# Kernel tuning notes

Hardware: AMD Instinct MI355X
Metric: run time of the kernel (lower is better)

## Reference

```python
import jax, jax.numpy as jnp
import numpy as np

SEQ, B, IN, H, L = 512, 64, 512, 512, 2


def setup_inputs() -> dict:
    key = jax.random.key(0)
    ks = jax.random.split(key, 9)
    s = 0.02
    x = jax.random.normal(ks[0], (SEQ, B, IN), dtype=jnp.float32)
    # torch Linear stores weight as [out, in]; stack per layer (IN == H so uniform)
    Wjx = jax.random.normal(ks[1], (L, H, IN), dtype=jnp.float32) * s
    bjx = jax.random.normal(ks[2], (L, H), dtype=jnp.float32) * s
    Wjh = jax.random.normal(ks[3], (L, H, H), dtype=jnp.float32) * s
    bjh = jax.random.normal(ks[4], (L, H), dtype=jnp.float32) * s
    Wkx = jax.random.normal(ks[5], (L, H, IN), dtype=jnp.float32) * s
    bkx = jax.random.normal(ks[6], (L, H), dtype=jnp.float32) * s
    Wkh = jax.random.normal(ks[7], (L, H, H), dtype=jnp.float32) * s
    bkh = jax.random.normal(ks[8], (L, H), dtype=jnp.float32) * s
    return {"x": x, "Wjx": Wjx, "bjx": bjx, "Wjh": Wjh, "bjh": bjh,
            "Wkx": Wkx, "bkx": bkx, "Wkh": Wkh, "bkh": bkh}


def reference(x, Wjx, bjx, Wjh, bjh, Wkx, bkx, Wkh, bkh):
    # x: [SEQ, B, IN]. Returns (outputs [SEQ, B, H], hidden [L, B, H]).
    L_, B_ = Wjx.shape[0], x.shape[1]
    h0 = jnp.zeros((L_, B_, Wjh.shape[1]), dtype=x.dtype)

    def step(hidden, xt):
        inp = xt  # [B, IN]
        new_h = []
        for l in range(L_):
            h = hidden[l]
            j = jax.nn.sigmoid(inp @ Wjx[l].T + bjx[l] + h @ Wjh[l].T + bjh[l])
            k = jax.nn.sigmoid(inp @ Wkx[l].T + bkx[l] + h @ Wkh[l].T + bkh[l])
            h = j * (1.0 - h) + (1.0 - k) * h
            new_h.append(h)
            inp = h
        return jnp.stack(new_h), inp

    hidden, outputs = jax.lax.scan(step, h0, x)
    return outputs, hidden
```

## Files before the change

### kernel.cpp

```cpp
#include <hip/hip_runtime.h>
#include <hip/hip_bf16.h>


#define SEQn 512
#define Bn   64
#define Hn   512
#define RING 8
#define BH   32768
#define TILE 8192

#define SPIN_MAIN 65536u

typedef __bf16 bf16x8 __attribute__((ext_vector_type(8)));
typedef float  f32x4  __attribute__((ext_vector_type(4)));
typedef unsigned u32;
typedef unsigned long long u64;

__device__ __forceinline__ u32 cload(const u32* p) {
    return __hip_atomic_load(p, __ATOMIC_RELAXED, __HIP_MEMORY_SCOPE_AGENT);
}
__device__ __forceinline__ void cstore(u32* p, u32 v) {
    __hip_atomic_store(p, v, __ATOMIC_RELAXED, __HIP_MEMORY_SCOPE_AGENT);
}
__device__ __forceinline__ unsigned short f2bf(float f) {
    u32 u = __float_as_uint(f);
    u += 0x7FFFu + ((u >> 16) & 1u);
    return (unsigned short)(u >> 16);
}
__device__ __forceinline__ bf16x8 cvt8(const float* p) {
    bf16x8 r;
#pragma unroll
    for (int i = 0; i < 8; ++i) r[i] = (__bf16)p[i];
    return r;
}

__global__ void __launch_bounds__(256, 1)
rnn_persistent(const float* __restrict__ x,
               const float* __restrict__ Wjx, const float* __restrict__ bjx,
               const float* __restrict__ Wjh, const float* __restrict__ bjh,
               const float* __restrict__ Wkx, const float* __restrict__ bkx,
               const float* __restrict__ Wkh, const float* __restrict__ bkh,
               float* __restrict__ out,
               u32* __restrict__ ring0,
               u32* __restrict__ ring1,
               u32* __restrict__ flags)
{
    const int wg    = blockIdx.x;
    const int layer = wg >> 7;
    const int id    = wg & 127;
    const int mg    = id >> 5;
    const int ng    = id & 31;
    const int tid   = threadIdx.x;
    const int wave  = tid >> 6;
    const int lane  = tid & 63;

    const int ucol = ng * 16 + (lane & 15);
    const int koff = (wave & 1) * 256 + ((lane >> 4) << 3);
    const float* wjsrc = ((wave < 2) ? Wjx : Wjh) + (size_t)layer * Hn * Hn + (size_t)ucol * Hn + koff;
    const float* wksrc = ((wave < 2) ? Wkx : Wkh) + (size_t)layer * Hn * Hn + (size_t)ucol * Hn + koff;
    bf16x8 wj[8], wk[8];
#pragma unroll
    for (int kt = 0; kt < 8; ++kt) {
        wj[kt] = cvt8(wjsrc + kt * 32);
        wk[kt] = cvt8(wksrc + kt * 32);
    }

    const int ml = tid >> 4;
    const int nu = tid & 15;
    const int ue = ng * 16 + nu;
    const int be = mg * 16 + ml;
    const float bje = bjx[layer * Hn + ue] + bjh[layer * Hn + ue];
    const float bke = bkx[layer * Hn + ue] + bkh[layer * Hn + ue];

    __shared__ float part[2][4][2][16][16];
    __shared__ char  xT[16384];
    __shared__ char  hT[16384];

    const int m = mg * 16 + (lane & 15);

    auto compute_global = [&](const float* Abase, int pb) {
        f32x4 aj = {0.f, 0.f, 0.f, 0.f}, ak = {0.f, 0.f, 0.f, 0.f};
        const float* arow = Abase + (size_t)m * Hn + koff;
#pragma unroll
        for (int kt = 0; kt < 8; ++kt) {
            bf16x8 af = cvt8(arow + kt * 32);
            aj = __builtin_amdgcn_mfma_f32_16x16x32_bf16(af, wj[kt], aj, 0, 0, 0);
            ak = __builtin_amdgcn_mfma_f32_16x16x32_bf16(af, wk[kt], ak, 0, 0, 0);
        }
#pragma unroll
        for (int r = 0; r < 4; ++r) {
            part[pb][wave][0][((lane >> 4) << 2) + r][lane & 15] = aj[r];
            part[pb][wave][1][((lane >> 4) << 2) + r][lane & 15] = ak[r];
        }
    };
    auto compute_lds = [&](const char* tile, int pb) {
        f32x4 aj = {0.f, 0.f, 0.f, 0.f}, ak = {0.f, 0.f, 0.f, 0.f};
        const int r       = lane & 15;
        const int cb      = ((wave & 1) << 8) + ((lane >> 4) << 3);
        const int swz     = (r & 7) << 4;
        const int rowbase = r << 10;
#pragma unroll
        for (int kt = 0; kt < 8; ++kt) {
            const int c = cb + kt * 32;
            bf16x8 af = *(const bf16x8*)(tile + ((rowbase + (c << 1)) ^ swz));
            aj = __builtin_amdgcn_mfma_f32_16x16x32_bf16(af, wj[kt], aj, 0, 0, 0);
            ak = __builtin_amdgcn_mfma_f32_16x16x32_bf16(af, wk[kt], ak, 0, 0, 0);
        }
#pragma unroll
        for (int r2 = 0; r2 < 4; ++r2) {
            part[pb][wave][0][((lane >> 4) << 2) + r2][lane & 15] = aj[r2];
            part[pb][wave][1][((lane >> 4) << 2) + r2][lane & 15] = ak[r2];
        }
    };
    auto zero_store = [&](int pb) {
#pragma unroll
        for (int r2 = 0; r2 < 4; ++r2) {
            part[pb][wave][0][((lane >> 4) << 2) + r2][lane & 15] = 0.f;
            part[pb][wave][1][((lane >> 4) << 2) + r2][lane & 15] = 0.f;
        }
    };
    auto stage_llc = [&](const u32* src, char* dstT, u32 want, bool sent) {
        if (sent) {
            const int p = tid & 31;
            const u32* sp = src + (((p & 15) << 9) | (p << 4) | 15);
            u32 it = 0;
            while (true) {
                u32 s = cload(sp);
                if (__all((s & 0xFFFFu) == want)) break;
                if (++it > SPIN_MAIN) break;
                __builtin_amdgcn_s_sleep(1);
            }
        }
        u32 v[32];
        u32 it = 0;
        while (true) {
            bool ok = true;
#pragma unroll
            for (int b = 0; b < 32; ++b) v[b] = cload(src + (b << 8) + tid);
#pragma unroll
            for (int b = 0; b < 32; ++b) ok &= ((v[b] & 0xFFFFu) == want);
            if (__all(ok)) break;
            if (++it > SPIN_MAIN) break;
            __builtin_amdgcn_s_sleep(1);
        }
#pragma unroll
        for (int b = 0; b < 32; ++b) {
            const int d = (b << 8) + tid, r = d >> 9;
            *(unsigned short*)(dstT + ((d << 1) ^ ((r & 7) << 4))) =
                (unsigned short)(v[b] >> 16);
        }
    };
    auto bpf_wait = [&](int want) {
        u32 it = 0;
        while (true) {
            int fv = (int)cload(flags + (mg << 5) + (lane & 31));
            if (__all(fv >= want)) break;
            if (++it > SPIN_MAIN) break;
            __builtin_amdgcn_s_sleep(1);
        }
    };

    float hprev = 0.f;

    for (int t = 0; t < SEQn; ++t) {
        const int pb    = t & 1;
        const int slot  = t & (RING - 1);
        const int pslot = (t - 1) & (RING - 1);
        const u32* hsrc = (layer == 0 ? ring0 : ring1)
                          + (size_t)pslot * BH + mg * TILE;
        const u32* xsrc = ring0 + (size_t)slot * BH + mg * TILE;

        if (layer == 0 && wave < 2)
            compute_global(x + (size_t)t * BH, pb);

        if (layer == 0) {
            if (t >= RING) bpf_wait(t - RING + 1);
            if (t > 0) stage_llc(hsrc, hT, (u32)t, true);
        } else {
            stage_llc(hsrc, hT, (u32)t, false);
            stage_llc(xsrc, xT, (u32)(t + 1), true);
        }
        __syncthreads();

        if (layer == 1 && tid == 0)
            cstore(flags + (mg << 5) + ng, (u32)(t + 1));

        if (layer == 0) { if (wave >= 2) { if (t > 0) compute_lds(hT, pb); else zero_store(pb); } }
        else            { if (wave < 2) compute_lds(xT, pb); else compute_lds(hT, pb); }
        __syncthreads();

        float sj = part[pb][0][0][ml][nu] + part[pb][1][0][ml][nu] +
                   part[pb][2][0][ml][nu] + part[pb][3][0][ml][nu] + bje;
        float sk = part[pb][0][1][ml][nu] + part[pb][1][1][ml][nu] +
                   part[pb][2][1][ml][nu] + part[pb][3][1][ml][nu] + bke;
        float jj = 1.f / (1.f + __expf(-sj));
        float kk = 1.f / (1.f + __expf(-sk));
        float hnew = jj * (1.f - hprev) + (1.f - kk) * hprev;
        hprev = hnew;

        u32 word = ((u32)f2bf(hnew) << 16) | (u32)(t + 1);
        cstore((layer == 0 ? ring0 : ring1) + (size_t)slot * BH + (size_t)be * Hn + ue, word);

        if (layer == 1)
            out[(size_t)t * BH + (size_t)be * Hn + ue] = hnew;
        if (t == SEQn - 1)
            out[(size_t)SEQn * BH + (size_t)layer * BH + (size_t)be * Hn + ue] = hnew;
    }
}

extern "C" void kernel_launch(void* const* d_in, const int* in_sizes, int n_in,
                              void* d_out, int out_size, void* d_ws, size_t ws_size,
                              hipStream_t stream) {
    (void)in_sizes; (void)n_in; (void)out_size; (void)ws_size;

    const float* x   = (const float*)d_in[0];
    const float* Wjx = (const float*)d_in[1];
    const float* bjx = (const float*)d_in[2];
    const float* Wjh = (const float*)d_in[3];
    const float* bjh = (const float*)d_in[4];
    const float* Wkx = (const float*)d_in[5];
    const float* bkx = (const float*)d_in[6];
    const float* Wkh = (const float*)d_in[7];
    const float* bkh = (const float*)d_in[8];
    float* out = (float*)d_out;

    char* ws = (char*)d_ws;
    u32* ring0 = (u32*)ws;
    u32* ring1 = (u32*)(ws + 1048576);
    u32* flags = (u32*)(ws + 2097152);

    hipMemsetAsync(ws, 0, 2097152 + 4096, stream);

    void* args[] = { (void*)&x, (void*)&Wjx, (void*)&bjx, (void*)&Wjh, (void*)&bjh,
                     (void*)&Wkx, (void*)&bkx, (void*)&Wkh, (void*)&bkh,
                     (void*)&out, (void*)&ring0, (void*)&ring1, (void*)&flags };
    hipError_t err = hipLaunchCooperativeKernel((void*)rnn_persistent, dim3(256),
                                                dim3(256), args, 0, stream);
    if (err != hipSuccess) {
        hipLaunchKernelGGL(rnn_persistent, dim3(256), dim3(256), 0, stream,
                           x, Wjx, bjx, Wjh, bjh, Wkx, bkx, Wkh, bkh,
                           out, ring0, ring1, flags);
    }
}
```

Before: 2.691 ms.

## Merge ring polling with backpressure check and poll both layer-1 inputs together

Doubles the inter-layer ring buffer depth so layer 0 can run further ahead of layer 1. The separate backpressure flag wait is folded into the layer-0 data polling loop, and the sentinel pre-spin before the full payload poll is removed. Layer 1 now polls its hidden-state and input rings in a single loop instead of two sequential ones, cutting serialized spin latency per timestep. In exchange it uses twice the workspace and raises the spin timeout; polling full payloads without a sentinel adds memory traffic while waiting.

```diff
diff --git a/kernel.cpp b/kernel.cpp
--- a/kernel.cpp
+++ b/kernel.cpp
@@ -5,16 +5,15 @@
 #define SEQn 512
 #define Bn   64
 #define Hn   512
-#define RING 8
+#define RING 16
 #define BH   32768
 #define TILE 8192
 
-#define SPIN_MAIN 65536u
+#define SPIN_MAIN 262144u
 
 typedef __bf16 bf16x8 __attribute__((ext_vector_type(8)));
 typedef float  f32x4  __attribute__((ext_vector_type(4)));
 typedef unsigned u32;
-typedef unsigned long long u64;
 
 __device__ __forceinline__ u32 cload(const u32* p) {
     return __hip_atomic_load(p, __ATOMIC_RELAXED, __HIP_MEMORY_SCOPE_AGENT);
@@ -119,26 +118,19 @@
             part[pb][wave][1][((lane >> 4) << 2) + r2][lane & 15] = 0.f;
         }
     };
-    auto stage_llc = [&](const u32* src, char* dstT, u32 want, bool sent) {
-        if (sent) {
-            const int p = tid & 31;
-            const u32* sp = src + (((p & 15) << 9) | (p << 4) | 15);
-            u32 it = 0;
-            while (true) {
-                u32 s = cload(sp);
-                if (__all((s & 0xFFFFu) == want)) break;
-                if (++it > SPIN_MAIN) break;
-                __builtin_amdgcn_s_sleep(1);
-            }
-        }
+
+    auto stage_l0 = [&](const u32* src, u32 want, int bwant) {
         u32 v[32];
+        const u32* fp = flags + (mg << 5) + (lane & 31);
         u32 it = 0;
         while (true) {
             bool ok = true;
 #pragma unroll
             for (int b = 0; b < 32; ++b) v[b] = cload(src + (b << 8) + tid);
+            int fv = (int)cload(fp);
 #pragma unroll
             for (int b = 0; b < 32; ++b) ok &= ((v[b] & 0xFFFFu) == want);
+            ok &= (fv >= bwant);
             if (__all(ok)) break;
             if (++it > SPIN_MAIN) break;
             __builtin_amdgcn_s_sleep(1);
@@ -146,17 +138,45 @@
 #pragma unroll
         for (int b = 0; b < 32; ++b) {
             const int d = (b << 8) + tid, r = d >> 9;
-            *(unsigned short*)(dstT + ((d << 1) ^ ((r & 7) << 4))) =
+            *(unsigned short*)(hT + ((d << 1) ^ ((r & 7) << 4))) =
                 (unsigned short)(v[b] >> 16);
         }
     };
-    auto bpf_wait = [&](int want) {
+    auto stage_l1 = [&](const u32* hsrc, const u32* xsrc, u32 hwant, u32 xwant) {
+        u32 vh[32], vx[32];
+        bool hok = false, xok = false;
         u32 it = 0;
         while (true) {
-            int fv = (int)cload(flags + (mg << 5) + (lane & 31));
-            if (__all(fv >= want)) break;
+            if (!hok) {
+#pragma unroll
+                for (int b = 0; b < 32; ++b) vh[b] = cload(hsrc + (b << 8) + tid);
+            }
+            if (!xok) {
+#pragma unroll
+                for (int b = 0; b < 32; ++b) vx[b] = cload(xsrc + (b << 8) + tid);
+            }
+            bool h2 = true, x2 = true;
+#pragma unroll
+            for (int b = 0; b < 32; ++b) h2 &= ((vh[b] & 0xFFFFu) == hwant);
+#pragma unroll
+            for (int b = 0; b < 32; ++b) x2 &= ((vx[b] & 0xFFFFu) == xwant);
+            hok = hok || __all(h2);
+            xok = xok || __all(x2);
+            if (hok && xok) break;
             if (++it > SPIN_MAIN) break;
             __builtin_amdgcn_s_sleep(1);
+        }
+#pragma unroll
+        for (int b = 0; b < 32; ++b) {
+            const int d = (b << 8) + tid, r = d >> 9;
+            *(unsigned short*)(hT + ((d << 1) ^ ((r & 7) << 4))) =
+                (unsigned short)(vh[b] >> 16);
+        }
+#pragma unroll
+        for (int b = 0; b < 32; ++b) {
+            const int d = (b << 8) + tid, r = d >> 9;
+            *(unsigned short*)(xT + ((d << 1) ^ ((r & 7) << 4))) =
+                (unsigned short)(vx[b] >> 16);
         }
     };
 
@@ -174,11 +194,9 @@
             compute_global(x + (size_t)t * BH, pb);
 
         if (layer == 0) {
-            if (t >= RING) bpf_wait(t - RING + 1);
-            if (t > 0) stage_llc(hsrc, hT, (u32)t, true);
+            if (t > 0) stage_l0(hsrc, (u32)t, t - RING + 1);
         } else {
-            stage_llc(hsrc, hT, (u32)t, false);
-            stage_llc(xsrc, xT, (u32)(t + 1), true);
+            stage_l1(hsrc, xsrc, (u32)t, (u32)(t + 1));
         }
         __syncthreads();
 
@@ -226,10 +244,10 @@
 
     char* ws = (char*)d_ws;
     u32* ring0 = (u32*)ws;
-    u32* ring1 = (u32*)(ws + 1048576);
-    u32* flags = (u32*)(ws + 2097152);
-
-    hipMemsetAsync(ws, 0, 2097152 + 4096, stream);
+    u32* ring1 = (u32*)(ws + 2097152);
+    u32* flags = (u32*)(ws + 4194304);
+
+    hipMemsetAsync(ws, 0, 4194304 + 4096, stream);
 
     void* args[] = { (void*)&x, (void*)&Wjx, (void*)&bjx, (void*)&Wjh, (void*)&bjh,
                      (void*)&Wkx, (void*)&bkx, (void*)&Wkh, (void*)&bkh,
```

After: 2.659 ms (median of 2 runs). About the same (-1.2%).
